# Kernel tuning notes

Measured on AMD Instinct MI355X. Metric: run time of the kernel, lower is better.

## Reference

```python
import jax, jax.numpy as jnp
import numpy as np
import math

N_EMBD = 1024
N_HEAD = 16
HEAD = N_EMBD // N_HEAD
LAMBDA_INIT = 0.8 - 0.6 * math.exp(-0.3 * (4 - 1))  # layer_idx=4
EPS = 1e-5


def setup_inputs() -> dict:
    key = jax.random.key(0)
    ks = jax.random.split(key, 12)
    s = 1.0 / math.sqrt(N_EMBD)
    inp = {
        "x": jax.random.normal(ks[0], (2, 2048, N_EMBD), dtype=jnp.float32),
        "q1_w": jax.random.normal(ks[1], (N_EMBD, N_EMBD), dtype=jnp.float32) * s,
        "q2_w": jax.random.normal(ks[2], (N_EMBD, N_EMBD), dtype=jnp.float32) * s,
        "k1_w": jax.random.normal(ks[3], (N_EMBD, N_EMBD), dtype=jnp.float32) * s,
        "k2_w": jax.random.normal(ks[4], (N_EMBD, N_EMBD), dtype=jnp.float32) * s,
        "v_w": jax.random.normal(ks[5], (N_EMBD, 2 * N_EMBD), dtype=jnp.float32) * s,
        "c_w": jax.random.normal(ks[6], (2 * N_EMBD, N_EMBD), dtype=jnp.float32) * (1.0 / math.sqrt(2 * N_EMBD)),
        "lambda_q1": jax.random.normal(ks[7], (N_HEAD, HEAD), dtype=jnp.float32) * 0.1,
        "lambda_k1": jax.random.normal(ks[8], (N_HEAD, HEAD), dtype=jnp.float32) * 0.1,
        "lambda_q2": jax.random.normal(ks[9], (N_HEAD, HEAD), dtype=jnp.float32) * 0.1,
        "lambda_k2": jax.random.normal(ks[10], (N_HEAD, HEAD), dtype=jnp.float32) * 0.1,
    }
    return inp


def reference(x, q1_w, q2_w, k1_w, k2_w, v_w, c_w,
              lambda_q1, lambda_k1, lambda_q2, lambda_k2):
    B, T, C = x.shape
    H, hs = N_HEAD, HEAD

    def heads(w, d):
        return (x @ w).reshape(B, T, H, d).transpose(0, 2, 1, 3)  # [B,H,T,d]

    q1 = heads(q1_w, hs)
    q2 = heads(q2_w, hs)
    k1 = heads(k1_w, hs)
    k2 = heads(k2_w, hs)
    v = heads(v_w, 2 * hs)  # [B,H,T,2*hs]

    scale = 1.0 / math.sqrt(hs)
    causal = jnp.tril(jnp.ones((T, T), dtype=bool))  # [T,T]
    neg = jnp.float32(-jnp.inf)

    att1 = jnp.einsum('bhqd,bhkd->bhqk', q1, k1) * scale
    att2 = jnp.einsum('bhqd,bhkd->bhqk', q2, k2) * scale
    att1 = jax.nn.softmax(jnp.where(causal, att1, neg), axis=-1)
    att2 = jax.nn.softmax(jnp.where(causal, att2, neg), axis=-1)

    lam1 = jnp.exp(jnp.sum(lambda_q1 * lambda_k1, axis=-1))  # [H]
    lam2 = jnp.exp(jnp.sum(lambda_q2 * lambda_k2, axis=-1))  # [H]
    lam = (lam1 - lam2 + LAMBDA_INIT)[None, :, None, None]

    att = att1 - lam * att2
    y = jnp.einsum('bhqk,bhkd->bhqd', att, v)  # [B,H,T,2*hs]

    # per-head LayerNorm over 2*hs, no affine
    mu = jnp.mean(y, axis=-1, keepdims=True)
    var = jnp.mean(jnp.square(y - mu), axis=-1, keepdims=True)
    y = (y - mu) / jnp.sqrt(var + EPS)
    y = y * (1.0 - LAMBDA_INIT)

    y = y.transpose(0, 2, 1, 3).reshape(B, T, 2 * C)
    return y @ c_w
```

## Files before the change

### kernel.cpp

```cpp
#include <hip/hip_runtime.h>
#include <cstdint>
#include <cstddef>

typedef __bf16 bf16;
typedef __bf16 bf16x8 __attribute__((ext_vector_type(8)));
typedef __bf16 bf16x4 __attribute__((ext_vector_type(4)));
typedef float f32x4 __attribute__((ext_vector_type(4)));

#define LAMBDA_INIT_F 0.5560582041556405f
#define ONE_MINUS_LI_F 0.4439417958443595f

static constexpr int T = 2048;
static constexpr int ROWQ = 6144;

__device__ __forceinline__ f32x4 mfma16(bf16x8 a, bf16x8 b, f32x4 c) {
  return __builtin_amdgcn_mfma_f32_16x16x32_bf16(a, b, c, 0, 0, 0);
}

__device__ __forceinline__ void gld16(const bf16* g, bf16* l) {
  __builtin_amdgcn_global_load_lds(
      (const __attribute__((address_space(1))) void*)g,
      (__attribute__((address_space(3))) void*)l, 16, 0, 0);
}


__global__ void cvt_f32_bf16(const float* __restrict__ src, bf16* __restrict__ dst, int n4) {
  int i = blockIdx.x * blockDim.x + threadIdx.x;
  if (i < n4) {
    float4 v = reinterpret_cast<const float4*>(src)[i];
    bf16x4 o;
    o[0] = (bf16)v.x; o[1] = (bf16)v.y; o[2] = (bf16)v.z; o[3] = (bf16)v.w;
    reinterpret_cast<bf16x4*>(dst)[i] = o;
  }
}

__global__ void transpose_cvt(const float* __restrict__ src, bf16* __restrict__ dst,
                              int K, int N) {
  __shared__ float t[32][33];
  int tx = threadIdx.x, ty = threadIdx.y;
  int n0 = blockIdx.x * 32, k0 = blockIdx.y * 32;
#pragma unroll
  for (int j = 0; j < 32; j += 8)
    t[ty + j][tx] = src[(size_t)(k0 + ty + j) * N + n0 + tx];
  __syncthreads();
#pragma unroll
  for (int j = 0; j < 32; j += 8)
    dst[(size_t)(n0 + ty + j) * K + k0 + tx] = (bf16)t[tx][ty + j];
}

__global__ void vtrans(const bf16* __restrict__ qkv, bf16* __restrict__ Vt) {
  __shared__ bf16 tile[64][72];
  const int tid = threadIdx.x;
  const int t0 = blockIdx.x * 64, dt = blockIdx.y, bh = blockIdx.z;
  const int b = bh >> 4, h = bh & 15;
#pragma unroll
  for (int i = 0; i < 2; ++i) {
    int S = tid + i * 256;
    int r = S >> 3, c = S & 7;
    *reinterpret_cast<bf16x8*>(&tile[r][c * 8]) =
        *reinterpret_cast<const bf16x8*>(
            &qkv[(size_t)(b * T + t0 + r) * ROWQ + 4096 + h * 128 + dt * 64 + c * 8]);
  }
  __syncthreads();
#pragma unroll
  for (int i = 0; i < 2; ++i) {
    int S = tid + i * 256;
    int dr = S >> 3, tc = S & 7;
    bf16x8 v;
#pragma unroll
    for (int j = 0; j < 8; ++j) v[j] = tile[tc * 8 + j][dr];
    *reinterpret_cast<bf16x8*>(
        &Vt[((size_t)bh * 128 + dt * 64 + dr) * 2048 + t0 + tc * 8]) = v;
  }
}


template <typename OutT>
__global__ __launch_bounds__(256, 2) void gemm_bt(const bf16* __restrict__ A,
                                                  const bf16* __restrict__ Bt,
                                                  OutT* __restrict__ C,
                                                  int M, int N, int K) {
  __shared__ __align__(16) bf16 As[2][128 * 64];
  __shared__ __align__(16) bf16 Bs[2][128 * 64];
  const int tid = threadIdx.x;
  const int lane = tid & 63;
  const int wv = tid >> 6;
  const int wr = wv >> 1, wc = wv & 1;
  const int bm = blockIdx.y * 128, bn = blockIdx.x * 128;
  const int lr = lane & 15, lg = lane >> 4;

  f32x4 acc[4][4] = {};
  const int KT = K >> 6;

#define STAGE_AB(buf, kk0)                                                      \
  do {                                                                          \
    _Pragma("unroll") for (int i_ = 0; i_ < 4; ++i_) {                          \
      int S_ = (i_ * 4 + wv) * 64 + lane;                                       \
      int rw_ = S_ >> 3;                                                        \
      int cg_ = (S_ & 7) ^ (rw_ & 7);                                           \
      gld16(&A[(size_t)(bm + rw_) * K + (kk0) + cg_ * 8], &As[buf][(i_ * 4 + wv) * 512]); \
      gld16(&Bt[(size_t)(bn + rw_) * K + (kk0) + cg_ * 8], &Bs[buf][(i_ * 4 + wv) * 512]); \
    }                                                                           \
  } while (0)

  STAGE_AB(0, 0);
  for (int kt = 0; kt < KT; ++kt) {
    const int cur = kt & 1;
    asm volatile("s_waitcnt vmcnt(0)" ::: "memory");
    __syncthreads();
    if (kt + 1 < KT) STAGE_AB(cur ^ 1, (kt + 1) * 64);
#pragma unroll
    for (int kh = 0; kh < 2; ++kh) {
      bf16x8 af[4], bfr[4];
#pragma unroll
      for (int m = 0; m < 4; ++m)
        af[m] = *reinterpret_cast<const bf16x8*>(
            &As[cur][(wr * 64 + m * 16 + lr) * 64 + (((kh * 4 + lg) ^ (lr & 7)) * 8)]);
#pragma unroll
      for (int n = 0; n < 4; ++n)
        bfr[n] = *reinterpret_cast<const bf16x8*>(
            &Bs[cur][(wc * 64 + n * 16 + lr) * 64 + (((kh * 4 + lg) ^ (lr & 7)) * 8)]);
#pragma unroll
      for (int m = 0; m < 4; ++m)
#pragma unroll
        for (int n = 0; n < 4; ++n)
          acc[m][n] = mfma16(af[m], bfr[n], acc[m][n]);
    }
  }
#undef STAGE_AB

#pragma unroll
  for (int m = 0; m < 4; ++m)
#pragma unroll
    for (int n = 0; n < 4; ++n)
#pragma unroll
      for (int r = 0; r < 4; ++r) {
        int row = bm + wr * 64 + m * 16 + lg * 4 + r;
        int col = bn + wc * 64 + n * 16 + lr;
        C[(size_t)row * N + col] = (OutT)acc[m][n][r];
      }
}


__global__ __launch_bounds__(256, 2) void diff_attn(const bf16* __restrict__ qkv,
                                                    const bf16* __restrict__ Vtg,
                                                    const float* __restrict__ lq1,
                                                    const float* __restrict__ lk1,
                                                    const float* __restrict__ lq2,
                                                    const float* __restrict__ lk2,
                                                    bf16* __restrict__ yln) {
  constexpr int LDP = 72;
  __shared__ __align__(16) bf16 K1s[2][64 * 64];
  __shared__ __align__(16) bf16 K2s[2][64 * 64];
  __shared__ __align__(16) bf16 Vs[2][128 * 64];
  __shared__ __align__(16) bf16 Ps[4][16 * LDP];

  const int fi = blockIdx.x;
  const int bh = blockIdx.y;
  const int b = bh >> 4, h = bh & 15;
  const int tid = threadIdx.x, lane = tid & 63, wv = tid >> 6;
  const int lr = lane & 15, lg = lane >> 4;
  const int qtA = 31 - fi;
  const int qtB = fi;

  const int q1c = h * 64;
  const int q2c = 1024 + h * 64;
  const int k1c = 2048 + h * 64;
  const int k2c = 3072 + h * 64;

  float a1 = lq1[h * 64 + lane] * lk1[h * 64 + lane];
  float a2 = lq2[h * 64 + lane] * lk2[h * 64 + lane];
#pragma unroll
  for (int m = 32; m >= 1; m >>= 1) {
    a1 += __shfl_xor(a1, m);
    a2 += __shfl_xor(a2, m);
  }
  const float lam = __expf(a1) - __expf(a2) + LAMBDA_INIT_F;

  bf16x8 onesf;
#pragma unroll
  for (int j = 0; j < 8; ++j) onesf[j] = (bf16)1.0f;

  bf16x8 q1fA[2], q2fA[2], q1fB[2], q2fB[2];
  {
    const bf16* qa = qkv + (size_t)(b * T + qtA * 64 + wv * 16 + lr) * ROWQ;
    const bf16* qb = qkv + (size_t)(b * T + qtB * 64 + wv * 16 + lr) * ROWQ;
#pragma unroll
    for (int kc = 0; kc < 2; ++kc) {
      q1fA[kc] = *reinterpret_cast<const bf16x8*>(qa + q1c + kc * 32 + lg * 8);
      q2fA[kc] = *reinterpret_cast<const bf16x8*>(qa + q2c + kc * 32 + lg * 8);
      q1fB[kc] = *reinterpret_cast<const bf16x8*>(qb + q1c + kc * 32 + lg * 8);
      q2fB[kc] = *reinterpret_cast<const bf16x8*>(qb + q2c + kc * 32 + lg * 8);
    }
  }

  f32x4 o1A[8] = {}, o2A[8] = {}, o1B[8] = {}, o2B[8] = {};
  f32x4 lA1 = {}, lA2 = {}, lB1 = {}, lB2 = {};

#define STAGE_KV(buf, tt0)                                                       \
  do {                                                                           \
    const bf16* kb_ = qkv + (size_t)(b * T + (tt0)) * ROWQ;                      \
    _Pragma("unroll") for (int i_ = 0; i_ < 2; ++i_) {                           \
      int S_ = (i_ * 4 + wv) * 64 + lane;                                        \
      int rw_ = S_ >> 3;                                                         \
      int cg_ = (S_ & 7) ^ (rw_ & 7);                                            \
      gld16(kb_ + (size_t)rw_ * ROWQ + k1c + cg_ * 8, &K1s[buf][(i_ * 4 + wv) * 512]); \
      gld16(kb_ + (size_t)rw_ * ROWQ + k2c + cg_ * 8, &K2s[buf][(i_ * 4 + wv) * 512]); \
    }                                                                            \
    _Pragma("unroll") for (int i_ = 0; i_ < 4; ++i_) {                           \
      int S_ = (i_ * 4 + wv) * 64 + lane;                                        \
      int dd_ = S_ >> 3;                                                         \
      int cg_ = (S_ & 7) ^ (dd_ & 7);                                            \
      gld16(Vtg + ((size_t)bh * 128 + dd_) * 2048 + (tt0) + cg_ * 8,             \
            &Vs[buf][(i_ * 4 + wv) * 512]);                                      \
    }                                                                            \
  } while (0)

#define ATT_STEP(q1f_, q2f_, o1_, o2_, l1_, l2_, edge_)                          \
  do {                                                                           \
    f32x4 s1_[4] = {}, s2_[4] = {};                                              \
    _Pragma("unroll") for (int n_ = 0; n_ < 4; ++n_) {                           \
      int krow_ = n_ * 16 + lr;                                                  \
      _Pragma("unroll") for (int kc_ = 0; kc_ < 2; ++kc_) {                      \
        bf16x8 kf1_ = *reinterpret_cast<const bf16x8*>(                          \
            &K1s[cur][krow_ * 64 + (((kc_ * 4 + lg) ^ (lr & 7)) * 8)]);          \
        bf16x8 kf2_ = *reinterpret_cast<const bf16x8*>(                          \
            &K2s[cur][krow_ * 64 + (((kc_ * 4 + lg) ^ (lr & 7)) * 8)]);          \
        s1_[n_] = mfma16(q1f_[kc_], kf1_, s1_[n_]);                              \
        s2_[n_] = mfma16(q2f_[kc_], kf2_, s2_[n_]);                              \
      }                                                                          \
    }                                                                            \
    _Pragma("unroll") for (int n_ = 0; n_ < 4; ++n_)                             \
    _Pragma("unroll") for (int r_ = 0; r_ < 4; ++r_) {                           \
      float e1_ = fmaf(s1_[n_][r_], 0.125f, -16.0f);                             \
      float e2_ = fmaf(s2_[n_][r_], 0.125f, -16.0f);                             \
      if (edge_) {                                                               \
        int qq_ = wv * 16 + lg * 4 + r_;                                         \
        int kk_ = n_ * 16 + lr;                                                  \
        if (kk_ > qq_) { e1_ = -1e4f; e2_ = -1e4f; }                             \
      }                                                                          \
      s1_[n_][r_] = __expf(e1_);                                                 \
      s2_[n_][r_] = __expf(e2_);                                                 \
    }                                                                            \
    bf16* Pw_ = &Ps[wv][0];                                                      \
    bf16x8 pa1_[2], pa2_[2];                                                     \
    _Pragma("unroll") for (int n_ = 0; n_ < 4; ++n_)                             \
    _Pragma("unroll") for (int r_ = 0; r_ < 4; ++r_)                             \
        Pw_[(lg * 4 + r_) * LDP + n_ * 16 + lr] = (bf16)s1_[n_][r_];             \
    _Pragma("unroll") for (int kc_ = 0; kc_ < 2; ++kc_)                          \
        pa1_[kc_] = *reinterpret_cast<const bf16x8*>(&Pw_[lr * LDP + kc_ * 32 + lg * 8]); \
    _Pragma("unroll") for (int n_ = 0; n_ < 4; ++n_)                             \
    _Pragma("unroll") for (int r_ = 0; r_ < 4; ++r_)                             \
        Pw_[(lg * 4 + r_) * LDP + n_ * 16 + lr] = (bf16)s2_[n_][r_];             \
    _Pragma("unroll") for (int kc_ = 0; kc_ < 2; ++kc_)                          \
        pa2_[kc_] = *reinterpret_cast<const bf16x8*>(&Pw_[lr * LDP + kc_ * 32 + lg * 8]); \
    _Pragma("unroll") for (int kc_ = 0; kc_ < 2; ++kc_) {                        \
      l1_ = mfma16(pa1_[kc_], onesf, l1_);                                       \
      l2_ = mfma16(pa2_[kc_], onesf, l2_);                                       \
      _Pragma("unroll") for (int nf_ = 0; nf_ < 8; ++nf_) {                      \
        int dd_ = nf_ * 16 + lr;                                                 \
        bf16x8 vb_ = *reinterpret_cast<const bf16x8*>(                           \
            &Vs[cur][dd_ * 64 + (((kc_ * 4 + lg) ^ (lr & 7)) * 8)]);             \
        o1_[nf_] = mfma16(pa1_[kc_], vb_, o1_[nf_]);                             \
        o2_[nf_] = mfma16(pa2_[kc_], vb_, o2_[nf_]);                             \
      }                                                                          \
    }                                                                            \
  } while (0)

  STAGE_KV(0, 0);
  for (int kt = 0; kt <= qtA; ++kt) {
    const int cur = kt & 1;
    asm volatile("s_waitcnt vmcnt(0)" ::: "memory");
    __syncthreads();
    if (kt < qtA) STAGE_KV(cur ^ 1, (kt + 1) * 64);
    ATT_STEP(q1fA, q2fA, o1A, o2A, lA1, lA2, (kt == qtA));
    if (kt <= qtB) ATT_STEP(q1fB, q2fB, o1B, o2B, lB1, lB2, (kt == qtB));
  }
#undef ATT_STEP
#undef STAGE_KV

#define ATT_EPI(o1_, o2_, l1_, l2_, qt_)                                         \
  do {                                                                           \
    float sum_[4] = {}, sq_[4] = {};                                             \
    float i1_[4], i2_[4];                                                        \
    _Pragma("unroll") for (int r_ = 0; r_ < 4; ++r_) {                           \
      i1_[r_] = 1.f / l1_[r_];                                                   \
      i2_[r_] = lam / l2_[r_];                                                   \
    }                                                                            \
    _Pragma("unroll") for (int nf_ = 0; nf_ < 8; ++nf_)                          \
    _Pragma("unroll") for (int r_ = 0; r_ < 4; ++r_) {                           \
      float v_ = o1_[nf_][r_] * i1_[r_] - o2_[nf_][r_] * i2_[r_];                \
      o1_[nf_][r_] = v_;                                                         \
      sum_[r_] += v_;                                                            \
      sq_[r_] += v_ * v_;                                                        \
    }                                                                            \
    _Pragma("unroll") for (int r_ = 0; r_ < 4; ++r_)                             \
    _Pragma("unroll") for (int mm_ = 8; mm_ >= 1; mm_ >>= 1) {                   \
      sum_[r_] += __shfl_xor(sum_[r_], mm_);                                     \
      sq_[r_] += __shfl_xor(sq_[r_], mm_);                                       \
    }                                                                            \
    _Pragma("unroll") for (int r_ = 0; r_ < 4; ++r_) {                           \
      float mu_ = sum_[r_] * (1.f / 128.f);                                      \
      float var_ = sq_[r_] * (1.f / 128.f) - mu_ * mu_;                          \
      float rs_ = rsqrtf(var_ + 1e-5f) * ONE_MINUS_LI_F;                         \
      int row_ = b * T + (qt_)*64 + wv * 16 + lg * 4 + r_;                       \
      bf16* orow_ = yln + (size_t)row_ * 2048 + h * 128;                         \
      _Pragma("unroll") for (int nf_ = 0; nf_ < 8; ++nf_)                        \
          orow_[nf_ * 16 + lr] = (bf16)((o1_[nf_][r_] - mu_) * rs_);             \
    }                                                                            \
  } while (0)

  ATT_EPI(o1A, o2A, lA1, lA2, qtA);
  ATT_EPI(o1B, o2B, lB1, lB2, qtB);
#undef ATT_EPI
}


extern "C" void kernel_launch(void* const* d_in, const int* in_sizes, int n_in,
                              void* d_out, int out_size, void* d_ws, size_t ws_size,
                              hipStream_t stream) {
  const float* x   = (const float*)d_in[0];
  const float* q1w = (const float*)d_in[1];
  const float* q2w = (const float*)d_in[2];
  const float* k1w = (const float*)d_in[3];
  const float* k2w = (const float*)d_in[4];
  const float* vw  = (const float*)d_in[5];
  const float* cw  = (const float*)d_in[6];
  const float* lq1 = (const float*)d_in[7];
  const float* lk1 = (const float*)d_in[8];
  const float* lq2 = (const float*)d_in[9];
  const float* lk2 = (const float*)d_in[10];
  float* out = (float*)d_out;

  char* ws = (char*)d_ws;
  bf16* qkv = (bf16*)(ws);
  bf16* Wt  = (bf16*)(ws + 50331648);
  bf16* xb  = (bf16*)(ws + 62914560);
  bf16* cwt = (bf16*)(ws + 71303168);
  bf16* yln = (bf16*)(ws + 75497472);
  bf16* Vt  = (bf16*)(ws + 50331648);

  cvt_f32_bf16<<<4096, 256, 0, stream>>>(x, xb, 4096 * 1024 / 4);

  dim3 tb(32, 8);
  transpose_cvt<<<dim3(32, 32), tb, 0, stream>>>(q1w, Wt,               1024, 1024);
  transpose_cvt<<<dim3(32, 32), tb, 0, stream>>>(q2w, Wt + 1024 * 1024, 1024, 1024);
  transpose_cvt<<<dim3(32, 32), tb, 0, stream>>>(k1w, Wt + 2048 * 1024, 1024, 1024);
  transpose_cvt<<<dim3(32, 32), tb, 0, stream>>>(k2w, Wt + 3072 * 1024, 1024, 1024);
  transpose_cvt<<<dim3(64, 32), tb, 0, stream>>>(vw,  Wt + 4096 * 1024, 1024, 2048);
  transpose_cvt<<<dim3(32, 64), tb, 0, stream>>>(cw,  cwt,              2048, 1024);

  gemm_bt<bf16><<<dim3(48, 32), 256, 0, stream>>>(xb, Wt, qkv, 4096, 6144, 1024);

  vtrans<<<dim3(32, 2, 32), 256, 0, stream>>>(qkv, Vt);

  diff_attn<<<dim3(16, 32), 256, 0, stream>>>(qkv, Vt, lq1, lk1, lq2, lk2, yln);

  gemm_bt<float><<<dim3(8, 32), 256, 0, stream>>>(yln, cwt, out, 4096, 1024, 2048);
}
```

Before: 218.5 us.

## Fuse weight transposes, add smaller-tile output GEMM, use exp2 and setprio in attention

Merges six weight transpose launches into a single kernel. Templates the GEMM on BM and runs the output projection with 64-row tiles so more blocks cover the device. In attention, folds log2e into the softmax scale to use exp2, reorders the query-tile mapping per batch, and raises wave priority around the compute step. Together these target launch overhead, tail underutilization and softmax instruction cost, at the price of a smaller per-block tile with lower operand reuse.

```diff
diff --git a/kernel.cpp b/kernel.cpp
--- a/kernel.cpp
+++ b/kernel.cpp
@@ -12,6 +12,8 @@
 
 static constexpr int T = 2048;
 static constexpr int ROWQ = 6144;
+#define C1_EXP2 0.18033688011116027f
+#define C0_EXP2 -23.083120654223414f
 
 __device__ __forceinline__ f32x4 mfma16(bf16x8 a, bf16x8 b, f32x4 c) {
   return __builtin_amdgcn_mfma_f32_16x16x32_bf16(a, b, c, 0, 0, 0);
@@ -34,11 +36,31 @@
   }
 }
 
-__global__ void transpose_cvt(const float* __restrict__ src, bf16* __restrict__ dst,
-                              int K, int N) {
+__global__ void transpose_all(const float* __restrict__ q1w, const float* __restrict__ q2w,
+                              const float* __restrict__ k1w, const float* __restrict__ k2w,
+                              const float* __restrict__ vw, const float* __restrict__ cw,
+                              bf16* __restrict__ Wt, bf16* __restrict__ cwt) {
   __shared__ float t[32][33];
-  int tx = threadIdx.x, ty = threadIdx.y;
-  int n0 = blockIdx.x * 32, k0 = blockIdx.y * 32;
+  const int id = blockIdx.x;
+  const float* src;
+  bf16* dst;
+  int K, N, bx, by;
+  if (id < 4096) {
+    int wsel = id >> 10, r = id & 1023;
+    src = (wsel == 0) ? q1w : (wsel == 1) ? q2w : (wsel == 2) ? k1w : k2w;
+    dst = Wt + (size_t)wsel * 1024 * 1024;
+    K = 1024; N = 1024; bx = r & 31; by = r >> 5;
+  } else if (id < 6144) {
+    int r = id - 4096;
+    src = vw; dst = Wt + (size_t)4096 * 1024;
+    K = 1024; N = 2048; bx = r & 63; by = r >> 6;
+  } else {
+    int r = id - 6144;
+    src = cw; dst = cwt;
+    K = 2048; N = 1024; bx = r & 31; by = r >> 5;
+  }
+  const int tx = threadIdx.x, ty = threadIdx.y;
+  const int n0 = bx * 32, k0 = by * 32;
 #pragma unroll
   for (int j = 0; j < 32; j += 8)
     t[ty + j][tx] = src[(size_t)(k0 + ty + j) * N + n0 + tx];
@@ -75,21 +97,24 @@
 }
 
 
-template <typename OutT>
-__global__ __launch_bounds__(256, 2) void gemm_bt(const bf16* __restrict__ A,
-                                                  const bf16* __restrict__ Bt,
-                                                  OutT* __restrict__ C,
-                                                  int M, int N, int K) {
-  __shared__ __align__(16) bf16 As[2][128 * 64];
+template <typename OutT, int BM>
+__global__ __launch_bounds__(256, BM == 128 ? 2 : 3) void gemm_bt(
+    const bf16* __restrict__ A, const bf16* __restrict__ Bt, OutT* __restrict__ C,
+    int M, int N, int K) {
+  constexpr int AIT = BM / 32;
+  constexpr int AN = (BM == 128) ? 4 : 2;
+  constexpr int WCN = (BM == 128) ? 64 : 32;
+  __shared__ __align__(16) bf16 As[2][BM * 64];
   __shared__ __align__(16) bf16 Bs[2][128 * 64];
   const int tid = threadIdx.x;
   const int lane = tid & 63;
   const int wv = tid >> 6;
-  const int wr = wv >> 1, wc = wv & 1;
-  const int bm = blockIdx.y * 128, bn = blockIdx.x * 128;
+  const int wr = (BM == 128) ? (wv >> 1) : 0;
+  const int wc = (BM == 128) ? (wv & 1) : wv;
+  const int bm = blockIdx.y * BM, bn = blockIdx.x * 128;
   const int lr = lane & 15, lg = lane >> 4;
 
-  f32x4 acc[4][4] = {};
+  f32x4 acc[4][AN] = {};
   const int KT = K >> 6;
 
 #define STAGE_AB(buf, kk0)                                                      \
@@ -98,7 +123,8 @@
       int S_ = (i_ * 4 + wv) * 64 + lane;                                       \
       int rw_ = S_ >> 3;                                                        \
       int cg_ = (S_ & 7) ^ (rw_ & 7);                                           \
-      gld16(&A[(size_t)(bm + rw_) * K + (kk0) + cg_ * 8], &As[buf][(i_ * 4 + wv) * 512]); \
+      if (i_ < AIT)                                                             \
+        gld16(&A[(size_t)(bm + rw_) * K + (kk0) + cg_ * 8], &As[buf][(i_ * 4 + wv) * 512]); \
       gld16(&Bt[(size_t)(bn + rw_) * K + (kk0) + cg_ * 8], &Bs[buf][(i_ * 4 + wv) * 512]); \
     }                                                                           \
   } while (0)
@@ -111,19 +137,19 @@
     if (kt + 1 < KT) STAGE_AB(cur ^ 1, (kt + 1) * 64);
 #pragma unroll
     for (int kh = 0; kh < 2; ++kh) {
-      bf16x8 af[4], bfr[4];
+      bf16x8 af[4], bfr[AN];
 #pragma unroll
       for (int m = 0; m < 4; ++m)
         af[m] = *reinterpret_cast<const bf16x8*>(
             &As[cur][(wr * 64 + m * 16 + lr) * 64 + (((kh * 4 + lg) ^ (lr & 7)) * 8)]);
 #pragma unroll
-      for (int n = 0; n < 4; ++n)
+      for (int n = 0; n < AN; ++n)
         bfr[n] = *reinterpret_cast<const bf16x8*>(
-            &Bs[cur][(wc * 64 + n * 16 + lr) * 64 + (((kh * 4 + lg) ^ (lr & 7)) * 8)]);
+            &Bs[cur][(wc * WCN + n * 16 + lr) * 64 + (((kh * 4 + lg) ^ (lr & 7)) * 8)]);
 #pragma unroll
       for (int m = 0; m < 4; ++m)
 #pragma unroll
-        for (int n = 0; n < 4; ++n)
+        for (int n = 0; n < AN; ++n)
           acc[m][n] = mfma16(af[m], bfr[n], acc[m][n]);
     }
   }
@@ -132,11 +158,11 @@
 #pragma unroll
   for (int m = 0; m < 4; ++m)
 #pragma unroll
-    for (int n = 0; n < 4; ++n)
+    for (int n = 0; n < AN; ++n)
 #pragma unroll
       for (int r = 0; r < 4; ++r) {
         int row = bm + wr * 64 + m * 16 + lg * 4 + r;
-        int col = bn + wc * 64 + n * 16 + lr;
+        int col = bn + wc * WCN + n * 16 + lr;
         C[(size_t)row * N + col] = (OutT)acc[m][n][r];
       }
 }
@@ -155,13 +181,14 @@
   __shared__ __align__(16) bf16 Vs[2][128 * 64];
   __shared__ __align__(16) bf16 Ps[4][16 * LDP];
 
-  const int fi = blockIdx.x;
+  const int x = blockIdx.x;
   const int bh = blockIdx.y;
   const int b = bh >> 4, h = bh & 15;
   const int tid = threadIdx.x, lane = tid & 63, wv = tid >> 6;
   const int lr = lane & 15, lg = lane >> 4;
-  const int qtA = 31 - fi;
-  const int qtB = fi;
+  const int u = b ? x : 15 - x;
+  const int qtA = 31 - u;
+  const int qtB = u;
 
   const int q1c = h * 64;
   const int q2c = 1024 + h * 64;
@@ -232,15 +259,15 @@
     }                                                                            \
     _Pragma("unroll") for (int n_ = 0; n_ < 4; ++n_)                             \
     _Pragma("unroll") for (int r_ = 0; r_ < 4; ++r_) {                           \
-      float e1_ = fmaf(s1_[n_][r_], 0.125f, -16.0f);                             \
-      float e2_ = fmaf(s2_[n_][r_], 0.125f, -16.0f);                             \
+      float e1_ = fmaf(s1_[n_][r_], C1_EXP2, C0_EXP2);                           \
+      float e2_ = fmaf(s2_[n_][r_], C1_EXP2, C0_EXP2);                           \
       if (edge_) {                                                               \
         int qq_ = wv * 16 + lg * 4 + r_;                                         \
         int kk_ = n_ * 16 + lr;                                                  \
-        if (kk_ > qq_) { e1_ = -1e4f; e2_ = -1e4f; }                             \
+        if (kk_ > qq_) { e1_ = -10000.f; e2_ = -10000.f; }                       \
       }                                                                          \
-      s1_[n_][r_] = __expf(e1_);                                                 \
-      s2_[n_][r_] = __expf(e2_);                                                 \
+      s1_[n_][r_] = exp2f(e1_);                                                  \
+      s2_[n_][r_] = exp2f(e2_);                                                  \
     }                                                                            \
     bf16* Pw_ = &Ps[wv][0];                                                      \
     bf16x8 pa1_[2], pa2_[2];                                                     \
@@ -273,8 +300,10 @@
     asm volatile("s_waitcnt vmcnt(0)" ::: "memory");
     __syncthreads();
     if (kt < qtA) STAGE_KV(cur ^ 1, (kt + 1) * 64);
+    __builtin_amdgcn_s_setprio(1);
     ATT_STEP(q1fA, q2fA, o1A, o2A, lA1, lA2, (kt == qtA));
     if (kt <= qtB) ATT_STEP(q1fB, q2fB, o1B, o2B, lB1, lB2, (kt == qtB));
+    __builtin_amdgcn_s_setprio(0);
   }
 #undef ATT_STEP
 #undef STAGE_KV
@@ -342,19 +371,13 @@
 
   cvt_f32_bf16<<<4096, 256, 0, stream>>>(x, xb, 4096 * 1024 / 4);
 
-  dim3 tb(32, 8);
-  transpose_cvt<<<dim3(32, 32), tb, 0, stream>>>(q1w, Wt,               1024, 1024);
-  transpose_cvt<<<dim3(32, 32), tb, 0, stream>>>(q2w, Wt + 1024 * 1024, 1024, 1024);
-  transpose_cvt<<<dim3(32, 32), tb, 0, stream>>>(k1w, Wt + 2048 * 1024, 1024, 1024);
-  transpose_cvt<<<dim3(32, 32), tb, 0, stream>>>(k2w, Wt + 3072 * 1024, 1024, 1024);
-  transpose_cvt<<<dim3(64, 32), tb, 0, stream>>>(vw,  Wt + 4096 * 1024, 1024, 2048);
-  transpose_cvt<<<dim3(32, 64), tb, 0, stream>>>(cw,  cwt,              2048, 1024);
-
-  gemm_bt<bf16><<<dim3(48, 32), 256, 0, stream>>>(xb, Wt, qkv, 4096, 6144, 1024);
+  transpose_all<<<8192, dim3(32, 8), 0, stream>>>(q1w, q2w, k1w, k2w, vw, cw, Wt, cwt);
+
+  gemm_bt<bf16, 128><<<dim3(48, 32), 256, 0, stream>>>(xb, Wt, qkv, 4096, 6144, 1024);
 
   vtrans<<<dim3(32, 2, 32), 256, 0, stream>>>(qkv, Vt);
 
   diff_attn<<<dim3(16, 32), 256, 0, stream>>>(qkv, Vt, lq1, lk1, lq2, lk2, yln);
 
-  gemm_bt<float><<<dim3(8, 32), 256, 0, stream>>>(yln, cwt, out, 4096, 1024, 2048);
-}
+  gemm_bt<float, 64><<<dim3(8, 64), 256, 0, stream>>>(yln, cwt, out, 4096, 1024, 2048);
+}
```

Result: no change. 219.3 us (+0.4%).
